# Performance work log

Measured on AMD Instinct MI355X. Metric: run time of the kernel, lower is better.

Reference implementation:

```python
import jax, jax.numpy as jnp
import numpy as np

DIM = 512
EDIM = 2 * DIM          # edim(=2) * dim
OUT_DIM = 512
KERNEL_SIZE = 4096
B, L = 4, 4096


def setup_inputs() -> dict:
    key = jax.random.key(0)
    k0, k1, k2, k3, k4 = jax.random.split(key, 5)
    embeddings = jax.random.normal(k0, (B, L, DIM), dtype=jnp.float32)
    logit_alpha = jax.random.uniform(k1, (EDIM,), minval=-3.0, maxval=3.0, dtype=jnp.float32)
    logit_delta = jax.random.uniform(k2, (EDIM,), minval=-3.0, maxval=3.0, dtype=jnp.float32)
    # xavier_uniform: U(-a, a), a = sqrt(6/(fan_in+fan_out))
    a_beta = float(np.sqrt(6.0 / (DIM + EDIM)))
    beta = jax.random.uniform(k3, (DIM, EDIM), minval=-a_beta, maxval=a_beta, dtype=jnp.float32)
    a_eta = float(np.sqrt(6.0 / (EDIM + OUT_DIM)))
    eta = jax.random.uniform(k4, (EDIM, OUT_DIM), minval=-a_eta, maxval=a_eta, dtype=jnp.float32)
    return {"embeddings": embeddings, "logit_alpha": logit_alpha,
            "logit_delta": logit_delta, "beta": beta, "eta": eta}


def reference(embeddings, logit_alpha, logit_delta, beta, eta):
    K = KERNEL_SIZE
    Lseq = embeddings.shape[1]
    # data-dependent EMA decay kernel: kernel[e, t] = p_e * q_e^t
    alpha = jax.nn.sigmoid(logit_alpha)[:, None]            # [E, 1]
    delta = jax.nn.sigmoid(logit_delta)[:, None]            # [E, 1]
    p = alpha
    q = 1.0 - alpha * delta
    len_range = jnp.arange(K, dtype=embeddings.dtype)[None, :]   # [1, K]
    kernel = p * jnp.exp(jnp.log(q) * len_range)            # [E, K]

    u = jnp.einsum('bld,de->ble', embeddings, beta)         # [B, L, E]
    u_T = jnp.swapaxes(u, -1, -2)                           # [B, E, L]

    # forward (causal) direction: flip kernel, full conv via FFT, slice at K-1
    kernel_f = jnp.flip(kernel, axis=-1)
    fft_dim = Lseq + K
    fft_dim = 1 << (fft_dim - 1).bit_length()               # next power of 2 (static)
    inp_fft = jnp.fft.rfft(u_T, n=fft_dim, axis=-1)
    ker_fft = jnp.fft.rfft(kernel_f, n=fft_dim, axis=-1)    # [E, fft_dim//2+1]
    out_full = jnp.fft.irfft(inp_fft * ker_fft, n=fft_dim, axis=-1)
    out_T = out_full[..., K - 1:K - 1 + Lseq].astype(embeddings.dtype)  # [B, E, L]

    out = jnp.swapaxes(out_T, -1, -2)                       # [B, L, E]
    return jnp.einsum('ble,eo->blo', out, eta)              # [B, L, out_dim]
```

## Files before the change

kernel.cpp:

```cpp
#include <hip/hip_runtime.h>
#include <hip/hip_bf16.h>

#define DIM      512
#define EDIM     1024
#define OUTD     512
#define BATCH    4
#define LSEQ     4096
#define MROWS    (BATCH * LSEQ)
#define NCHUNK   64
#define CHUNK    (LSEQ / NCHUNK)

typedef __attribute__((ext_vector_type(8))) __bf16 bf16x8;
typedef __attribute__((ext_vector_type(4))) float  f32x4;

static __device__ __forceinline__ ushort f2b(float f) {
    uint x = __float_as_uint(f);
    x += 0x7fff + ((x >> 16) & 1);
    return (ushort)(x >> 16);
}
static __device__ __forceinline__ float b2f(ushort u) {
    return __uint_as_float(((uint)u) << 16);
}
static __device__ __forceinline__ float sigmoidf(float x) {
    return 1.0f / (1.0f + expf(-x));
}

__global__ void prep_cvt_kernel(const float* __restrict__ emb,
                                ushort* __restrict__ a16,
                                const float* __restrict__ beta,
                                const float* __restrict__ eta,
                                const float* __restrict__ la,
                                const float* __restrict__ ld,
                                ushort* __restrict__ betaT,
                                ushort* __restrict__ etaT,
                                float* __restrict__ p,
                                float* __restrict__ q) {
    int blk = blockIdx.x;
    if (blk < 8192) {
        int i = blk * 256 + threadIdx.x;
        float4 v = ((const float4*)emb)[i];
        ushort4 o;
        o.x = f2b(v.x); o.y = f2b(v.y); o.z = f2b(v.z); o.w = f2b(v.w);
        ((ushort4*)a16)[i] = o;
    } else {
        int i = (blk - 8192) * 256 + threadIdx.x;
        if (i < EDIM * DIM) {
            int n = i / DIM, k = i - n * DIM;
            betaT[i] = f2b(beta[(size_t)k * EDIM + n]);
        }
        if (i < OUTD * EDIM) {
            int o = i / EDIM, e = i - o * EDIM;
            etaT[i] = f2b(eta[(size_t)e * OUTD + o]);
        }
        if (i < EDIM) {
            float a = sigmoidf(la[i]);
            float d = sigmoidf(ld[i]);
            p[i] = a;
            q[i] = 1.0f - a * d;
        }
    }
}

template <int OUT_BF16, int DO_AGG>
__global__ __launch_bounds__(256) void gemm_bt(const ushort* __restrict__ A,
                                               const ushort* __restrict__ Bt,
                                               void* __restrict__ Cv,
                                               const float* __restrict__ qv,
                                               float* __restrict__ aggp,
                                               int M, int N, int K,
                                               int ncolShift) {
    __shared__ ushort smem[16384];
    const int tid  = threadIdx.x;
    const int lane = tid & 63;
    const int wid  = tid >> 6;
    const int wr   = wid >> 1, wc = wid & 1;
    const int l15  = lane & 15;
    const int l4   = lane >> 4;

    const int nwg   = gridDim.x;
    const int chunkw = nwg >> 3;
    const int flat  = (blockIdx.x & 7) * chunkw + (blockIdx.x >> 3);
    const int rowBase = (flat >> ncolShift) << 7;
    const int colBase = (flat & ((1 << ncolShift) - 1)) << 7;

    f32x4 acc[4][4] = {};

    const int nkb = K >> 6;
    for (int kb = 0; kb < nkb; ++kb) {
        #pragma unroll
        for (int r = 0; r < 4; ++r) {
            int c     = r * 256 + tid;
            int row   = c >> 3;
            int col16 = (c & 7) ^ (row & 7);
            const ushort* ga = A  + (size_t)(rowBase + row) * K + kb * 64 + col16 * 8;
            __builtin_amdgcn_global_load_lds(
                (const __attribute__((address_space(1))) void*)ga,
                (__attribute__((address_space(3))) void*)((char*)smem + c * 16),
                16, 0, 0);
            const ushort* gb = Bt + (size_t)(colBase + row) * K + kb * 64 + col16 * 8;
            __builtin_amdgcn_global_load_lds(
                (const __attribute__((address_space(1))) void*)gb,
                (__attribute__((address_space(3))) void*)((char*)smem + 16384 + c * 16),
                16, 0, 0);
        }
        __syncthreads();

        #pragma unroll
        for (int kk = 0; kk < 2; ++kk) {
            bf16x8 af[4], bfr[4];
            #pragma unroll
            for (int m = 0; m < 4; ++m) {
                int row   = wr * 64 + m * 16 + l15;
                int kbyte = kk * 64 + l4 * 16;
                int addr  = row * 128 + (kbyte ^ ((row & 7) << 4));
                af[m] = *(const bf16x8*)((const char*)smem + addr);
            }
            #pragma unroll
            for (int n = 0; n < 4; ++n) {
                int row   = wc * 64 + n * 16 + l15;
                int kbyte = kk * 64 + l4 * 16;
                int addr  = 16384 + row * 128 + (kbyte ^ ((row & 7) << 4));
                bfr[n] = *(const bf16x8*)((const char*)smem + addr);
            }
            #pragma unroll
            for (int m = 0; m < 4; ++m)
                #pragma unroll
                for (int n = 0; n < 4; ++n)
                    acc[m][n] = __builtin_amdgcn_mfma_f32_16x16x32_bf16(
                        af[m], bfr[n], acc[m][n], 0, 0, 0);
        }
        __syncthreads();
    }

    #pragma unroll
    for (int m = 0; m < 4; ++m)
        #pragma unroll
        for (int n = 0; n < 4; ++n)
            #pragma unroll
            for (int r = 0; r < 4; ++r) {
                int row = rowBase + wr * 64 + m * 16 + l4 * 4 + r;
                int col = colBase + wc * 64 + n * 16 + l15;
                if (OUT_BF16)
                    ((ushort*)Cv)[(size_t)row * N + col] = f2b(acc[m][n][r]);
                else
                    ((float*)Cv)[(size_t)row * N + col] = acc[m][n][r];
            }

    if (DO_AGG) {
        const int bidx     = rowBase >> 12;
        const int chunkIdx = ((rowBase & 4095) >> 6) + wr;
        #pragma unroll
        for (int n = 0; n < 4; ++n) {
            int col = colBase + wc * 64 + n * 16 + l15;
            float qe = qv[col];
            float q2 = qe * qe, q4 = q2 * q2, q8 = q4 * q4, q16 = q8 * q8;
            float P = 0.0f;
            #pragma unroll
            for (int m = 3; m >= 0; --m) {
                f32x4 a = acc[m][n];
                float pm = ((a[3] * qe + a[2]) * qe + a[1]) * qe + a[0];
                P = P * q16 + pm;
            }
            float ql4 = (l4 & 1 ? q4 : 1.0f) * (l4 & 2 ? q8 : 1.0f);
            P *= ql4;
            P += __shfl_xor(P, 16, 64);
            P += __shfl_xor(P, 32, 64);
            if (l4 == 0)
                aggp[(((bidx << 6) | chunkIdx) << 10) + col] = P;
        }
    }
}

__global__ void scan_apply_kernel(ushort* __restrict__ u,
                                  const float* __restrict__ pv,
                                  const float* __restrict__ qv,
                                  const float* __restrict__ agg) {
    int t = blockIdx.x * blockDim.x + threadIdx.x;
    int e0 = (t & 511) * 2;
    int c  = (t >> 9) & 63;
    int b  = t >> 15;
    float2 qe2 = *(const float2*)(qv + e0);
    float2 pe2 = *(const float2*)(pv + e0);
    float qe[2] = {qe2.x, qe2.y};
    float pe[2] = {pe2.x, pe2.y};
    float qL[2], S[2], w[2];
    #pragma unroll
    for (int k = 0; k < 2; ++k) {
        float x = qe[k];
        #pragma unroll
        for (int s = 0; s < 6; ++s) x *= x;
        qL[k] = x; S[k] = 0.0f; w[k] = 1.0f;
    }
    for (int cp = c + 1; cp < NCHUNK; ++cp) {
        float2 a = *(const float2*)(agg + (((b << 6) | cp) << 10) + e0);
        S[0] += w[0] * a.x;  w[0] *= qL[0];
        S[1] += w[1] * a.y;  w[1] *= qL[1];
    }
    ushort* up = u + ((size_t)(b * LSEQ + c * CHUNK) << 10) + e0;
    #pragma unroll 4
    for (int j = CHUNK - 1; j >= 0; --j) {
        ushort2 uv = *(ushort2*)(up + (size_t)j * EDIM);
        S[0] = b2f(uv.x) + qe[0] * S[0];
        S[1] = b2f(uv.y) + qe[1] * S[1];
        ushort2 ov;
        ov.x = f2b(pe[0] * S[0]);
        ov.y = f2b(pe[1] * S[1]);
        *(ushort2*)(up + (size_t)j * EDIM) = ov;
    }
}

extern "C" void kernel_launch(void* const* d_in, const int* in_sizes, int n_in,
                              void* d_out, int out_size, void* d_ws, size_t ws_size,
                              hipStream_t stream) {
    const float* emb  = (const float*)d_in[0];
    const float* la   = (const float*)d_in[1];
    const float* ld   = (const float*)d_in[2];
    const float* beta = (const float*)d_in[3];
    const float* eta  = (const float*)d_in[4];

    char* ws = (char*)d_ws;
    ushort* a16   = (ushort*)(ws);
    ushort* betaT = (ushort*)(ws + 16777216);
    ushort* etaT  = (ushort*)(ws + 17825792);
    ushort* u     = (ushort*)(ws + 18874368);
    float*  p     = (float*) (ws + 52428800);
    float*  q     = (float*) (ws + 52432896);
    float*  agg   = (float*) (ws + 52436992);

    prep_cvt_kernel<<<dim3(10240), dim3(256), 0, stream>>>(
        emb, a16, beta, eta, la, ld, betaT, etaT, p, q);

    gemm_bt<1, 1><<<dim3((MROWS / 128) * (EDIM / 128)), dim3(256), 0, stream>>>(
        a16, betaT, (void*)u, q, agg, MROWS, EDIM, DIM, 3);

    scan_apply_kernel<<<dim3(512), dim3(256), 0, stream>>>(u, p, q, agg);

    gemm_bt<0, 0><<<dim3((MROWS / 128) * (OUTD / 128)), dim3(256), 0, stream>>>(
        u, etaT, d_out, nullptr, nullptr, MROWS, OUTD, EDIM, 2);
}
```

Before: 87.28 us.

## Use 256x256-tile double-buffered direct-to-LDS GEMM for the first projection

Replaces the 128x128 GEMM for embeddings×beta with a new 256x256-tile kernel of 512 threads. It loads global memory straight into swizzled LDS through global_load_lds, double-buffers K-tiles in 128KB of dynamic shared memory, and interleaves LDS fragment loads with MFMA phases using barriers and setprio. The goal is more data reuse per tile and overlap of loads with compute. The chunk-aggregate epilogue moves into the new kernel, and the second GEMM keeps the old path. The grid shrinks to 256 workgroups, which may underfill the device, and the large LDS allocation limits occupancy.

Result: faster. 83.74 us (-4.1%).

```diff
diff --git a/kernel.cpp b/kernel.cpp
--- a/kernel.cpp
+++ b/kernel.cpp
@@ -61,12 +61,183 @@
     }
 }
 
-template <int OUT_BF16, int DO_AGG>
+#define MFMA_BF16 __builtin_amdgcn_mfma_f32_16x16x32_bf16
+template <int KDIM, int NSHIFT, int OUT_BF16, int DO_AGG>
+__global__ __launch_bounds__(512, 2) void gemm256(const ushort* __restrict__ A,
+                                                  const ushort* __restrict__ Bt,
+                                                  void* __restrict__ Cv,
+                                                  const float* __restrict__ qv,
+                                                  float* __restrict__ aggp,
+                                                  int N) {
+    extern __shared__ __align__(16) char smem[];
+    const int tid  = threadIdx.x;
+    const int lane = tid & 63;
+    const int wid  = tid >> 6;
+    const int wr   = wid >> 2;
+    const int wc   = wid & 3;
+    const int l15  = lane & 15;
+    const int l4   = lane >> 4;
+
+    const int nwg  = gridDim.x;
+    const int flat = ((int)blockIdx.x & 7) * (nwg >> 3) + ((int)blockIdx.x >> 3);
+    const int rowBase = (flat >> NSHIFT) << 8;
+    const int colBase = (flat & ((1 << NSHIFT) - 1)) << 8;
+
+    const int row0  = tid >> 3;
+    const int col16 = (tid & 7) ^ (row0 & 7);
+    const ushort* gA0 = A  + (size_t)(rowBase + row0) * KDIM + col16 * 8;
+    const ushort* gB0 = Bt + (size_t)(colBase + row0) * KDIM + col16 * 8;
+    const int ldsOff = tid * 16;
+
+    const int sw   = (l15 & 7) << 4;
+    const int aRow = (wr * 128 + l15) * 128;
+    const int bRow = 32768 + (wc * 64 + l15) * 128;
+    const int a0 = aRow + ((l4 * 16) ^ sw);
+    const int a1 = aRow + ((64 + l4 * 16) ^ sw);
+    const int b0 = bRow + ((l4 * 16) ^ sw);
+    const int b1 = bRow + ((64 + l4 * 16) ^ sw);
+
+    f32x4 acc[8][4] = {};
+    bf16x8 af[4][2], bfr[4][2];
+
+    const int NT = KDIM >> 6;
+
+    auto STAGE = [&](int t) {
+        const int boff = (t & 1) << 16;
+        const size_t koff = (size_t)t * 64;
+        #pragma unroll
+        for (int i = 0; i < 4; ++i)
+            __builtin_amdgcn_global_load_lds(
+                (const __attribute__((address_space(1))) void*)(gA0 + (size_t)i * 64 * KDIM + koff),
+                (__attribute__((address_space(3))) void*)(smem + boff + i * 8192 + ldsOff),
+                16, 0, 0);
+        #pragma unroll
+        for (int i = 0; i < 4; ++i)
+            __builtin_amdgcn_global_load_lds(
+                (const __attribute__((address_space(1))) void*)(gB0 + (size_t)i * 64 * KDIM + koff),
+                (__attribute__((address_space(3))) void*)(smem + boff + 32768 + i * 8192 + ldsOff),
+                16, 0, 0);
+    };
+
+    STAGE(0);
+    asm volatile("s_waitcnt vmcnt(0)" ::: "memory");
+    __builtin_amdgcn_s_barrier();
+
+    for (int t = 0; t < NT; ++t) {
+        const char* sm = smem + ((t & 1) << 16);
+        if (t + 1 < NT) STAGE(t + 1);
+        #pragma unroll
+        for (int m = 0; m < 4; ++m) {
+            af[m][0] = *(const bf16x8*)(sm + a0 + m * 2048);
+            af[m][1] = *(const bf16x8*)(sm + a1 + m * 2048);
+        }
+        #pragma unroll
+        for (int n = 0; n < 2; ++n) {
+            bfr[n][0] = *(const bf16x8*)(sm + b0 + n * 2048);
+            bfr[n][1] = *(const bf16x8*)(sm + b1 + n * 2048);
+        }
+        __builtin_amdgcn_s_barrier();
+        __builtin_amdgcn_s_setprio(1);
+        #pragma unroll
+        for (int m = 0; m < 4; ++m)
+            #pragma unroll
+            for (int n = 0; n < 2; ++n) {
+                acc[m][n] = MFMA_BF16(af[m][0], bfr[n][0], acc[m][n], 0, 0, 0);
+                acc[m][n] = MFMA_BF16(af[m][1], bfr[n][1], acc[m][n], 0, 0, 0);
+            }
+        __builtin_amdgcn_s_setprio(0);
+        __builtin_amdgcn_s_barrier();
+        #pragma unroll
+        for (int n = 2; n < 4; ++n) {
+            bfr[n][0] = *(const bf16x8*)(sm + b0 + n * 2048);
+            bfr[n][1] = *(const bf16x8*)(sm + b1 + n * 2048);
+        }
+        __builtin_amdgcn_s_barrier();
+        __builtin_amdgcn_s_setprio(1);
+        #pragma unroll
+        for (int m = 0; m < 4; ++m)
+            #pragma unroll
+            for (int n = 2; n < 4; ++n) {
+                acc[m][n] = MFMA_BF16(af[m][0], bfr[n][0], acc[m][n], 0, 0, 0);
+                acc[m][n] = MFMA_BF16(af[m][1], bfr[n][1], acc[m][n], 0, 0, 0);
+            }
+        __builtin_amdgcn_s_setprio(0);
+        __builtin_amdgcn_s_barrier();
+        #pragma unroll
+        for (int m = 0; m < 4; ++m) {
+            af[m][0] = *(const bf16x8*)(sm + a0 + (m + 4) * 2048);
+            af[m][1] = *(const bf16x8*)(sm + a1 + (m + 4) * 2048);
+        }
+        __builtin_amdgcn_s_barrier();
+        __builtin_amdgcn_s_setprio(1);
+        #pragma unroll
+        for (int m = 0; m < 4; ++m)
+            #pragma unroll
+            for (int n = 0; n < 2; ++n) {
+                acc[m + 4][n] = MFMA_BF16(af[m][0], bfr[n][0], acc[m + 4][n], 0, 0, 0);
+                acc[m + 4][n] = MFMA_BF16(af[m][1], bfr[n][1], acc[m + 4][n], 0, 0, 0);
+            }
+        __builtin_amdgcn_s_setprio(0);
+        __builtin_amdgcn_s_barrier();
+        __builtin_amdgcn_s_setprio(1);
+        #pragma unroll
+        for (int m = 0; m < 4; ++m)
+            #pragma unroll
+            for (int n = 2; n < 4; ++n) {
+                acc[m + 4][n] = MFMA_BF16(af[m][0], bfr[n][0], acc[m + 4][n], 0, 0, 0);
+                acc[m + 4][n] = MFMA_BF16(af[m][1], bfr[n][1], acc[m + 4][n], 0, 0, 0);
+            }
+        __builtin_amdgcn_s_setprio(0);
+        asm volatile("s_waitcnt vmcnt(0)" ::: "memory");
+        __builtin_amdgcn_s_barrier();
+    }
+
+    #pragma unroll
+    for (int m = 0; m < 8; ++m)
+        #pragma unroll
+        for (int n = 0; n < 4; ++n)
+            #pragma unroll
+            for (int r = 0; r < 4; ++r) {
+                int row = rowBase + wr * 128 + m * 16 + l4 * 4 + r;
+                int col = colBase + wc * 64 + n * 16 + l15;
+                if (OUT_BF16)
+                    ((ushort*)Cv)[(size_t)row * N + col] = f2b(acc[m][n][r]);
+                else
+                    ((float*)Cv)[(size_t)row * N + col] = acc[m][n][r];
+            }
+
+    if (DO_AGG) {
+        const int bidx = rowBase >> 12;
+        const int chunkBase = ((rowBase & 4095) >> 6) + wr * 2;
+        #pragma unroll
+        for (int h = 0; h < 2; ++h) {
+            #pragma unroll
+            for (int n = 0; n < 4; ++n) {
+                int col = colBase + wc * 64 + n * 16 + l15;
+                float qe = qv[col];
+                float q2 = qe * qe, q4 = q2 * q2, q8 = q4 * q4, q16 = q8 * q8;
+                float P = 0.0f;
+                #pragma unroll
+                for (int m = 3; m >= 0; --m) {
+                    f32x4 a = acc[h * 4 + m][n];
+                    float pm = ((a[3] * qe + a[2]) * qe + a[1]) * qe + a[0];
+                    P = P * q16 + pm;
+                }
+                float ql4 = (l4 & 1 ? q4 : 1.0f) * (l4 & 2 ? q8 : 1.0f);
+                P *= ql4;
+                P += __shfl_xor(P, 16, 64);
+                P += __shfl_xor(P, 32, 64);
+                if (l4 == 0)
+                    aggp[(((bidx << 6) | (chunkBase + h)) << 10) + col] = P;
+            }
+        }
+    }
+}
+
+template <int OUT_BF16>
 __global__ __launch_bounds__(256) void gemm_bt(const ushort* __restrict__ A,
                                                const ushort* __restrict__ Bt,
                                                void* __restrict__ Cv,
-                                               const float* __restrict__ qv,
-                                               float* __restrict__ aggp,
                                                int M, int N, int K,
                                                int ncolShift) {
     __shared__ ushort smem[16384];
@@ -145,30 +316,6 @@
                 else
                     ((float*)Cv)[(size_t)row * N + col] = acc[m][n][r];
             }
-
-    if (DO_AGG) {
-        const int bidx     = rowBase >> 12;
-        const int chunkIdx = ((rowBase & 4095) >> 6) + wr;
-        #pragma unroll
-        for (int n = 0; n < 4; ++n) {
-            int col = colBase + wc * 64 + n * 16 + l15;
-            float qe = qv[col];
-            float q2 = qe * qe, q4 = q2 * q2, q8 = q4 * q4, q16 = q8 * q8;
-            float P = 0.0f;
-            #pragma unroll
-            for (int m = 3; m >= 0; --m) {
-                f32x4 a = acc[m][n];
-                float pm = ((a[3] * qe + a[2]) * qe + a[1]) * qe + a[0];
-                P = P * q16 + pm;
-            }
-            float ql4 = (l4 & 1 ? q4 : 1.0f) * (l4 & 2 ? q8 : 1.0f);
-            P *= ql4;
-            P += __shfl_xor(P, 16, 64);
-            P += __shfl_xor(P, 32, 64);
-            if (l4 == 0)
-                aggp[(((bidx << 6) | chunkIdx) << 10) + col] = P;
-        }
-    }
 }
 
 __global__ void scan_apply_kernel(ushort* __restrict__ u,
@@ -227,14 +374,17 @@
     float*  q     = (float*) (ws + 52432896);
     float*  agg   = (float*) (ws + 52436992);
 
+    (void)hipFuncSetAttribute((const void*)gemm256<512, 2, 1, 1>,
+                              hipFuncAttributeMaxDynamicSharedMemorySize, 131072);
+
     prep_cvt_kernel<<<dim3(10240), dim3(256), 0, stream>>>(
         emb, a16, beta, eta, la, ld, betaT, etaT, p, q);
 
-    gemm_bt<1, 1><<<dim3((MROWS / 128) * (EDIM / 128)), dim3(256), 0, stream>>>(
-        a16, betaT, (void*)u, q, agg, MROWS, EDIM, DIM, 3);
+    gemm256<512, 2, 1, 1><<<dim3(256), dim3(512), 131072, stream>>>(
+        a16, betaT, (void*)u, q, agg, EDIM);
 
     scan_apply_kernel<<<dim3(512), dim3(256), 0, stream>>>(u, p, q, agg);
 
-    gemm_bt<0, 0><<<dim3((MROWS / 128) * (OUTD / 128)), dim3(256), 0, stream>>>(
-        u, etaT, d_out, nullptr, nullptr, MROWS, OUTD, EDIM, 2);
-}
+    gemm_bt<0><<<dim3((MROWS / 128) * (OUTD / 128)), dim3(256), 0, stream>>>(
+        u, etaT, d_out, MROWS, OUTD, EDIM, 2);
+}
```

## Fuse fp32-to-bf16 conversion into GEMM and double-buffer 128x256 tiles

Applied to the files above, without the earlier changes.

Removes the separate embedding conversion pass: the first GEMM now loads fp32 embeddings into registers, converts them to bf16 and writes them into LDS itself. Both GEMMs move to a 128x256 tile with 8 waves, double-buffered LDS, prefetch of the next K tile during MFMA work, and s_setprio around the MFMA blocks. The goal is to drop a full read and write of the activation tensor and to hide global load latency. In exchange it uses 96KB of LDS per block and more registers, which limits occupancy and makes the schedule more fragile.

Result: slower. 89.63 us (+2.7%).

```diff
diff --git a/kernel.cpp b/kernel.cpp
--- a/kernel.cpp
+++ b/kernel.cpp
@@ -25,111 +25,165 @@
     return 1.0f / (1.0f + expf(-x));
 }
 
-__global__ void prep_cvt_kernel(const float* __restrict__ emb,
-                                ushort* __restrict__ a16,
-                                const float* __restrict__ beta,
-                                const float* __restrict__ eta,
-                                const float* __restrict__ la,
-                                const float* __restrict__ ld,
-                                ushort* __restrict__ betaT,
-                                ushort* __restrict__ etaT,
-                                float* __restrict__ p,
-                                float* __restrict__ q) {
-    int blk = blockIdx.x;
-    if (blk < 8192) {
-        int i = blk * 256 + threadIdx.x;
-        float4 v = ((const float4*)emb)[i];
-        ushort4 o;
-        o.x = f2b(v.x); o.y = f2b(v.y); o.z = f2b(v.z); o.w = f2b(v.w);
-        ((ushort4*)a16)[i] = o;
-    } else {
-        int i = (blk - 8192) * 256 + threadIdx.x;
-        if (i < EDIM * DIM) {
-            int n = i / DIM, k = i - n * DIM;
-            betaT[i] = f2b(beta[(size_t)k * EDIM + n]);
-        }
-        if (i < OUTD * EDIM) {
-            int o = i / EDIM, e = i - o * EDIM;
-            etaT[i] = f2b(eta[(size_t)e * OUTD + o]);
-        }
-        if (i < EDIM) {
-            float a = sigmoidf(la[i]);
-            float d = sigmoidf(ld[i]);
-            p[i] = a;
-            q[i] = 1.0f - a * d;
-        }
-    }
-}
-
-template <int OUT_BF16, int DO_AGG>
-__global__ __launch_bounds__(256) void gemm_bt(const ushort* __restrict__ A,
-                                               const ushort* __restrict__ Bt,
-                                               void* __restrict__ Cv,
-                                               const float* __restrict__ qv,
-                                               float* __restrict__ aggp,
-                                               int M, int N, int K,
-                                               int ncolShift) {
-    __shared__ ushort smem[16384];
+__global__ void prep_kernel(const float* __restrict__ beta,
+                            const float* __restrict__ eta,
+                            const float* __restrict__ la,
+                            const float* __restrict__ ld,
+                            ushort* __restrict__ betaT,
+                            ushort* __restrict__ etaT,
+                            float* __restrict__ p,
+                            float* __restrict__ q) {
+    int i = blockIdx.x * blockDim.x + threadIdx.x;
+    if (i < EDIM * DIM) {
+        int n = i / DIM, k = i - n * DIM;
+        betaT[i] = f2b(beta[(size_t)k * EDIM + n]);
+    }
+    if (i < OUTD * EDIM) {
+        int o = i / EDIM, e = i - o * EDIM;
+        etaT[i] = f2b(eta[(size_t)e * OUTD + o]);
+    }
+    if (i < EDIM) {
+        float a = sigmoidf(la[i]);
+        float d = sigmoidf(ld[i]);
+        p[i] = a;
+        q[i] = 1.0f - a * d;
+    }
+}
+
+#define MFMA_BF16 __builtin_amdgcn_mfma_f32_16x16x32_bf16
+#define LDSBUF 49152
+
+template <int KDIM, int NSHIFT, int A_FP32, int OUT_BF16, int DO_AGG>
+__global__ __launch_bounds__(512, 2) void gemm128x256(
+        const void* __restrict__ Av, const ushort* __restrict__ Bt,
+        void* __restrict__ Cv, const float* __restrict__ qv,
+        float* __restrict__ aggp, int N) {
+    extern __shared__ __align__(16) char smem[];
     const int tid  = threadIdx.x;
     const int lane = tid & 63;
     const int wid  = tid >> 6;
-    const int wr   = wid >> 1, wc = wid & 1;
+    const int wr   = wid >> 2;
+    const int wc   = wid & 3;
     const int l15  = lane & 15;
     const int l4   = lane >> 4;
 
-    const int nwg   = gridDim.x;
-    const int chunkw = nwg >> 3;
-    const int flat  = (blockIdx.x & 7) * chunkw + (blockIdx.x >> 3);
-    const int rowBase = (flat >> ncolShift) << 7;
-    const int colBase = (flat & ((1 << ncolShift) - 1)) << 7;
-
+    const int nwg  = gridDim.x;
+    const int flat = ((int)blockIdx.x & 7) * (nwg >> 3) + ((int)blockIdx.x >> 3);
+    const int rowBase = (flat >> NSHIFT) << 7;
+    const int colBase = (flat & ((1 << NSHIFT) - 1)) << 8;
+
+    const int sw   = (l15 & 7) << 4;
+    const int aRowB = (wr * 64 + l15) * 128;
+    const int bRowB = 16384 + (wc * 64 + l15) * 128;
+    const int ra0 = aRowB + ((l4 * 16) ^ sw);
+    const int ra1 = aRowB + ((64 + l4 * 16) ^ sw);
+    const int rb0 = bRowB + ((l4 * 16) ^ sw);
+    const int rb1 = bRowB + ((64 + l4 * 16) ^ sw);
+
+    const int srow = tid >> 3;
+    const int scol = (tid & 7) ^ (srow & 7);
+    const ushort* gB0 = Bt + (size_t)(colBase + srow) * KDIM + scol * 8;
+    const ushort* gA0b = (const ushort*)Av + (size_t)(rowBase + srow) * KDIM + scol * 8;
+    const float*  gA0f = (const float*)Av + (size_t)(rowBase + (tid >> 2)) * KDIM + (tid & 3) * 16;
+
+    float4 aReg[4];
+    bf16x8 af[4][2], bfr[4][2];
     f32x4 acc[4][4] = {};
 
-    const int nkb = K >> 6;
-    for (int kb = 0; kb < nkb; ++kb) {
-        #pragma unroll
-        for (int r = 0; r < 4; ++r) {
-            int c     = r * 256 + tid;
-            int row   = c >> 3;
-            int col16 = (c & 7) ^ (row & 7);
-            const ushort* ga = A  + (size_t)(rowBase + row) * K + kb * 64 + col16 * 8;
+    auto ISSUE = [&](int t) {
+        const int boff = (t & 1) * LDSBUF;
+        const int koff = t * 64;
+        if (A_FP32) {
+            const float4* src = (const float4*)(gA0f + koff);
+            #pragma unroll
+            for (int i = 0; i < 4; ++i) aReg[i] = src[i];
+        } else {
+            #pragma unroll
+            for (int i = 0; i < 2; ++i)
+                __builtin_amdgcn_global_load_lds(
+                    (const __attribute__((address_space(1))) void*)(gA0b + (size_t)i * 64 * KDIM + koff),
+                    (__attribute__((address_space(3))) void*)(smem + boff + i * 8192 + tid * 16),
+                    16, 0, 0);
+        }
+        #pragma unroll
+        for (int i = 0; i < 4; ++i)
             __builtin_amdgcn_global_load_lds(
-                (const __attribute__((address_space(1))) void*)ga,
-                (__attribute__((address_space(3))) void*)((char*)smem + c * 16),
+                (const __attribute__((address_space(1))) void*)(gB0 + (size_t)i * 64 * KDIM + koff),
+                (__attribute__((address_space(3))) void*)(smem + boff + 16384 + i * 8192 + tid * 16),
                 16, 0, 0);
-            const ushort* gb = Bt + (size_t)(colBase + row) * K + kb * 64 + col16 * 8;
-            __builtin_amdgcn_global_load_lds(
-                (const __attribute__((address_space(1))) void*)gb,
-                (__attribute__((address_space(3))) void*)((char*)smem + 16384 + c * 16),
-                16, 0, 0);
-        }
-        __syncthreads();
-
-        #pragma unroll
-        for (int kk = 0; kk < 2; ++kk) {
-            bf16x8 af[4], bfr[4];
-            #pragma unroll
-            for (int m = 0; m < 4; ++m) {
-                int row   = wr * 64 + m * 16 + l15;
-                int kbyte = kk * 64 + l4 * 16;
-                int addr  = row * 128 + (kbyte ^ ((row & 7) << 4));
-                af[m] = *(const bf16x8*)((const char*)smem + addr);
-            }
-            #pragma unroll
-            for (int n = 0; n < 4; ++n) {
-                int row   = wc * 64 + n * 16 + l15;
-                int kbyte = kk * 64 + l4 * 16;
-                int addr  = 16384 + row * 128 + (kbyte ^ ((row & 7) << 4));
-                bfr[n] = *(const bf16x8*)((const char*)smem + addr);
-            }
-            #pragma unroll
-            for (int m = 0; m < 4; ++m)
-                #pragma unroll
-                for (int n = 0; n < 4; ++n)
-                    acc[m][n] = __builtin_amdgcn_mfma_f32_16x16x32_bf16(
-                        af[m], bfr[n], acc[m][n], 0, 0, 0);
-        }
-        __syncthreads();
+    };
+
+    auto STAGE_WRITE = [&](int t) {
+        const int boff = (t & 1) * LDSBUF;
+        const int row  = tid >> 2;
+        const int swr  = (row & 7) << 4;
+        char* base = smem + boff + row * 128;
+        uint w[8];
+        #pragma unroll
+        for (int i = 0; i < 4; ++i) {
+            w[i * 2]     = (uint)f2b(aReg[i].x) | ((uint)f2b(aReg[i].y) << 16);
+            w[i * 2 + 1] = (uint)f2b(aReg[i].z) | ((uint)f2b(aReg[i].w) << 16);
+        }
+        uint4 v0 = {w[0], w[1], w[2], w[3]};
+        uint4 v1 = {w[4], w[5], w[6], w[7]};
+        *(uint4*)(base + (((tid & 3) * 32)      ^ swr)) = v0;
+        *(uint4*)(base + (((tid & 3) * 32 + 16) ^ swr)) = v1;
+    };
+
+    ISSUE(0);
+    if (A_FP32) {
+        asm volatile("s_waitcnt vmcnt(4)" ::: "memory");
+        STAGE_WRITE(0);
+    }
+    asm volatile("s_waitcnt vmcnt(0) lgkmcnt(0)" ::: "memory");
+    __builtin_amdgcn_s_barrier();
+
+    const int NT = KDIM >> 6;
+    for (int t = 0; t < NT; ++t) {
+        const char* sm = smem + (t & 1) * LDSBUF;
+        if (t + 1 < NT) ISSUE(t + 1);
+        #pragma unroll
+        for (int m = 0; m < 4; ++m) {
+            af[m][0] = *(const bf16x8*)(sm + ra0 + m * 2048);
+            af[m][1] = *(const bf16x8*)(sm + ra1 + m * 2048);
+        }
+        #pragma unroll
+        for (int n = 0; n < 2; ++n) {
+            bfr[n][0] = *(const bf16x8*)(sm + rb0 + n * 2048);
+            bfr[n][1] = *(const bf16x8*)(sm + rb1 + n * 2048);
+        }
+        __builtin_amdgcn_s_barrier();
+        __builtin_amdgcn_s_setprio(1);
+        #pragma unroll
+        for (int m = 0; m < 4; ++m)
+            #pragma unroll
+            for (int n = 0; n < 2; ++n) {
+                acc[m][n] = MFMA_BF16(af[m][0], bfr[n][0], acc[m][n], 0, 0, 0);
+                acc[m][n] = MFMA_BF16(af[m][1], bfr[n][1], acc[m][n], 0, 0, 0);
+            }
+        __builtin_amdgcn_s_setprio(0);
+        __builtin_amdgcn_s_barrier();
+        if (A_FP32 && t + 1 < NT) {
+            asm volatile("s_waitcnt vmcnt(4)" ::: "memory");
+            STAGE_WRITE(t + 1);
+        }
+        #pragma unroll
+        for (int n = 2; n < 4; ++n) {
+            bfr[n][0] = *(const bf16x8*)(sm + rb0 + n * 2048);
+            bfr[n][1] = *(const bf16x8*)(sm + rb1 + n * 2048);
+        }
+        __builtin_amdgcn_s_barrier();
+        __builtin_amdgcn_s_setprio(1);
+        #pragma unroll
+        for (int m = 0; m < 4; ++m)
+            #pragma unroll
+            for (int n = 2; n < 4; ++n) {
+                acc[m][n] = MFMA_BF16(af[m][0], bfr[n][0], acc[m][n], 0, 0, 0);
+                acc[m][n] = MFMA_BF16(af[m][1], bfr[n][1], acc[m][n], 0, 0, 0);
+            }
+        __builtin_amdgcn_s_setprio(0);
+        asm volatile("s_waitcnt vmcnt(0) lgkmcnt(0)" ::: "memory");
+        __builtin_amdgcn_s_barrier();
     }
 
     #pragma unroll
@@ -219,22 +273,26 @@
     const float* eta  = (const float*)d_in[4];
 
     char* ws = (char*)d_ws;
-    ushort* a16   = (ushort*)(ws);
-    ushort* betaT = (ushort*)(ws + 16777216);
-    ushort* etaT  = (ushort*)(ws + 17825792);
-    ushort* u     = (ushort*)(ws + 18874368);
-    float*  p     = (float*) (ws + 52428800);
-    float*  q     = (float*) (ws + 52432896);
-    float*  agg   = (float*) (ws + 52436992);
-
-    prep_cvt_kernel<<<dim3(10240), dim3(256), 0, stream>>>(
-        emb, a16, beta, eta, la, ld, betaT, etaT, p, q);
-
-    gemm_bt<1, 1><<<dim3((MROWS / 128) * (EDIM / 128)), dim3(256), 0, stream>>>(
-        a16, betaT, (void*)u, q, agg, MROWS, EDIM, DIM, 3);
+    ushort* betaT = (ushort*)(ws);
+    ushort* etaT  = (ushort*)(ws + 1048576);
+    ushort* u     = (ushort*)(ws + 2097152);
+    float*  p     = (float*) (ws + 35651584);
+    float*  q     = (float*) (ws + 35655680);
+    float*  agg   = (float*) (ws + 35659776);
+
+    (void)hipFuncSetAttribute((const void*)gemm128x256<512, 2, 1, 1, 1>,
+                              hipFuncAttributeMaxDynamicSharedMemorySize, 98304);
+    (void)hipFuncSetAttribute((const void*)gemm128x256<1024, 1, 0, 0, 0>,
+                              hipFuncAttributeMaxDynamicSharedMemorySize, 98304);
+
+    prep_kernel<<<dim3(2048), dim3(256), 0, stream>>>(beta, eta, la, ld,
+                                                      betaT, etaT, p, q);
+
+    gemm128x256<512, 2, 1, 1, 1><<<dim3(512), dim3(512), 98304, stream>>>(
+        emb, betaT, (void*)u, q, agg, EDIM);
 
     scan_apply_kernel<<<dim3(512), dim3(256), 0, stream>>>(u, p, q, agg);
 
-    gemm_bt<0, 0><<<dim3((MROWS / 128) * (OUTD / 128)), dim3(256), 0, stream>>>(
-        u, etaT, d_out, nullptr, nullptr, MROWS, OUTD, EDIM, 2);
-}
+    gemm128x256<1024, 1, 0, 0, 0><<<dim3(256), dim3(512), 98304, stream>>>(
+        u, etaT, d_out, nullptr, nullptr, OUTD);
+}
```
